# Performance work log

Measured on AMD Instinct MI355X. Metric: run time of the kernel, lower is better.

The kernel has to match this reference:

```python
import jax, jax.numpy as jnp
import numpy as np

N_HEAD = 8
N_INPUTS = 2
N_EMBD = 256
B, T1, T2 = 4, 8192, 8192


def setup_inputs() -> dict:
    key = jax.random.key(0)
    ks = jax.random.split(key, 8)
    s = 1.0 / np.sqrt(N_EMBD)
    return {
        "x": jax.random.normal(ks[0], (B, T1, N_EMBD), dtype=jnp.float32),
        "y": jax.random.normal(ks[1], (N_INPUTS, B, T2, N_EMBD), dtype=jnp.float32),
        "Wq": jax.random.normal(ks[2], (N_EMBD, N_EMBD), dtype=jnp.float32) * s,
        "bq": jnp.zeros((N_EMBD,), dtype=jnp.float32),
        "Wk": jax.random.normal(ks[3], (N_INPUTS, N_EMBD, N_EMBD), dtype=jnp.float32) * s,
        "bk": jnp.zeros((N_INPUTS, N_EMBD), dtype=jnp.float32),
        "Wv": jax.random.normal(ks[4], (N_INPUTS, N_EMBD, N_EMBD), dtype=jnp.float32) * s,
        "bv": jnp.zeros((N_INPUTS, N_EMBD), dtype=jnp.float32),
        "Wp": jax.random.normal(ks[5], (N_EMBD, N_EMBD), dtype=jnp.float32) * s,
        "bp": jnp.zeros((N_EMBD,), dtype=jnp.float32),
    }


def _split_heads(t):
    # [B, T, C] -> [B, H, T, d]
    Bt, Tt, C = t.shape
    return t.reshape(Bt, Tt, N_HEAD, C // N_HEAD).transpose(0, 2, 1, 3)


def reference(x, y, Wq, bq, Wk, bk, Wv, bv, Wp, bp):
    Bx, T, C = x.shape
    q = jax.nn.softmax(_split_heads(x @ Wq + bq), axis=-1)  # [B,H,T1,d]
    out = q  # faithful to original: out initialized to q
    for i in range(N_INPUTS):
        k = jax.nn.softmax(_split_heads(y[i] @ Wk[i] + bk[i]), axis=-1)  # [B,H,T2,d]
        v = _split_heads(y[i] @ Wv[i] + bv[i])                            # [B,H,T2,d]
        k_cumsum = k.sum(axis=-2, keepdims=True)                          # [B,H,1,d]
        D_inv = 1.0 / (q * k_cumsum).sum(axis=-1, keepdims=True)          # [B,H,T1,1]
        kv = jnp.einsum('bhtd,bhte->bhde', k, v)                          # [B,H,d,d]
        out = out + jnp.einsum('bhnd,bhde->bhne', q, kv) * D_inv
    # b h n d -> b n (h d)
    out = out.transpose(0, 2, 1, 3).reshape(Bx, T, C)
    return out @ Wp + bp
```

## Files before the change

### kernel.cpp

```cpp
#include <hip/hip_runtime.h>
#include <math.h>

#define NHEAD 8
#define CEMB  256
#define NIN   2
#define BB    4
#define TT    8192

typedef __attribute__((ext_vector_type(8))) short short8;
typedef __attribute__((ext_vector_type(4))) float f32x4;
typedef __attribute__((ext_vector_type(16))) float f32x16;

__device__ __forceinline__ unsigned short f2bf(float f) {
    union { float f; unsigned u; } v; v.f = f;
    unsigned u = v.u;
    return (unsigned short)((u + 0x7fffu + ((u >> 16) & 1u)) >> 16);
}
__device__ __forceinline__ float bf2f(unsigned short s) {
    union { unsigned u; float f; } v; v.u = ((unsigned)s) << 16;
    return v.f;
}

__global__ __launch_bounds__(256) void prep_w(const float* __restrict__ Wq,
    const float* __restrict__ Wk, const float* __restrict__ Wv,
    const float* __restrict__ Wp, unsigned short* __restrict__ wsb)
{
    int gid = blockIdx.x * 256 + threadIdx.x;
    int m = gid >> 16;
    int idx = gid & 65535;
    int n = idx >> 8, k = idx & 255;
    const float* src; unsigned short* dst;
    switch (m) {
        case 0: src = Wq;          dst = wsb;          break;
        case 1: src = Wk;          dst = wsb + 65536;  break;
        case 2: src = Wk + 65536;  dst = wsb + 131072; break;
        case 3: src = Wv;          dst = wsb + 196608; break;
        case 4: src = Wv + 65536;  dst = wsb + 262144; break;
        default: src = Wp;         dst = wsb + 327680; break;
    }
    dst[n * 256 + k] = f2bf(src[k * 256 + n]);
}

__global__ __launch_bounds__(512, 4) void passA(const float* __restrict__ y,
    const float* __restrict__ bk, const float* __restrict__ bv,
    const unsigned short* __restrict__ Wkt, const unsigned short* __restrict__ Wvt,
    float* __restrict__ part)
{
    __shared__ unsigned short ytile[64][256];
    __shared__ unsigned short tr[8][32][64];

    const int i = blockIdx.z, b = blockIdx.y, x0 = blockIdx.x;
    const int tid = threadIdx.x;
    const int wid = tid >> 6, lane = tid & 63;
    const int lg = lane >> 4, li = lane & 15;
    const int l31 = lane & 31, hk = lane >> 5;
    const int h = wid, lm = li & 7;

    const float bk0 = bk[i * CEMB + h * 32 + li];
    const float bk1 = bk[i * CEMB + h * 32 + 16 + li];
    const float bv0 = bv[i * CEMB + h * 32 + li];
    const float bv1 = bv[i * CEMB + h * 32 + 16 + li];

    f32x16 kvacc = {};
    float ksa0 = 0.f, ksa1 = 0.f;

    for (int iter = 0; iter < 2; ++iter) {
        __syncthreads();
        const int row0 = x0 * 128 + iter * 64;
        const float* yb = y + ((size_t)(i * BB + b) * TT + row0) * CEMB;
        #pragma unroll
        for (int j = 0; j < 8; ++j) {
            int idx = tid + j * 512;
            int r = idx >> 6, c4 = (idx & 63) << 2;
            int sw = ((((c4 >> 3) ^ (r & 7)) << 3) | (c4 & 7));
            float4 v4 = *(const float4*)&yb[(size_t)r * CEMB + c4];
            ushort4 p; p.x = f2bf(v4.x); p.y = f2bf(v4.y); p.z = f2bf(v4.z); p.w = f2bf(v4.w);
            *(ushort4*)&ytile[r][sw] = p;
        }
        __syncthreads();

        f32x4 acc[4][2];
        #pragma unroll
        for (int rt = 0; rt < 4; ++rt) { acc[rt][0] = (f32x4){}; acc[rt][1] = (f32x4){}; }
        {
            const unsigned short* wk0 = Wkt + ((size_t)(i * 256 + h * 32 + li)) * 256 + lg * 8;
            const unsigned short* wk1 = wk0 + 16 * 256;
            #pragma unroll 2
            for (int ks = 0; ks < 8; ++ks) {
                const int sw8 = (((4 * ks + lg) ^ lm) << 3);
                short8 a0 = *(const short8*)&ytile[li][sw8];
                short8 a1 = *(const short8*)&ytile[16 + li][sw8];
                short8 a2 = *(const short8*)&ytile[32 + li][sw8];
                short8 a3 = *(const short8*)&ytile[48 + li][sw8];
                short8 f0 = *(const short8*)(wk0 + ks * 32);
                short8 f1 = *(const short8*)(wk1 + ks * 32);
                acc[0][0] = __builtin_amdgcn_mfma_f32_16x16x32_bf16(a0, f0, acc[0][0], 0, 0, 0);
                acc[0][1] = __builtin_amdgcn_mfma_f32_16x16x32_bf16(a0, f1, acc[0][1], 0, 0, 0);
                acc[1][0] = __builtin_amdgcn_mfma_f32_16x16x32_bf16(a1, f0, acc[1][0], 0, 0, 0);
                acc[1][1] = __builtin_amdgcn_mfma_f32_16x16x32_bf16(a1, f1, acc[1][1], 0, 0, 0);
                acc[2][0] = __builtin_amdgcn_mfma_f32_16x16x32_bf16(a2, f0, acc[2][0], 0, 0, 0);
                acc[2][1] = __builtin_amdgcn_mfma_f32_16x16x32_bf16(a2, f1, acc[2][1], 0, 0, 0);
                acc[3][0] = __builtin_amdgcn_mfma_f32_16x16x32_bf16(a3, f0, acc[3][0], 0, 0, 0);
                acc[3][1] = __builtin_amdgcn_mfma_f32_16x16x32_bf16(a3, f1, acc[3][1], 0, 0, 0);
            }
        }
        #pragma unroll
        for (int rt = 0; rt < 4; ++rt) {
            float kq0[4], kq1[4];
            #pragma unroll
            for (int reg = 0; reg < 4; ++reg) {
                float l0 = acc[rt][0][reg] + bk0;
                float l1 = acc[rt][1][reg] + bk1;
                float m = fmaxf(l0, l1);
                m = fmaxf(m, __shfl_xor(m, 1, 16));
                m = fmaxf(m, __shfl_xor(m, 2, 16));
                m = fmaxf(m, __shfl_xor(m, 4, 16));
                m = fmaxf(m, __shfl_xor(m, 8, 16));
                float e0 = __expf(l0 - m), e1 = __expf(l1 - m);
                float s = e0 + e1;
                s += __shfl_xor(s, 1, 16);
                s += __shfl_xor(s, 2, 16);
                s += __shfl_xor(s, 4, 16);
                s += __shfl_xor(s, 8, 16);
                float isv = 1.f / s;
                kq0[reg] = e0 * isv; kq1[reg] = e1 * isv;
                ksa0 += kq0[reg]; ksa1 += kq1[reg];
            }
            const int wof = ((((2 * rt + (lg >> 1)) ^ lm) << 3) | ((lg & 1) << 2));
            ushort4 p;
            p.x = f2bf(kq0[0]); p.y = f2bf(kq0[1]); p.z = f2bf(kq0[2]); p.w = f2bf(kq0[3]);
            *(ushort4*)&tr[wid][li][wof] = p;
            p.x = f2bf(kq1[0]); p.y = f2bf(kq1[1]); p.z = f2bf(kq1[2]); p.w = f2bf(kq1[3]);
            *(ushort4*)&tr[wid][16 + li][wof] = p;
        }
        #pragma unroll
        for (int rt = 0; rt < 4; ++rt) { acc[rt][0] = (f32x4){}; acc[rt][1] = (f32x4){}; }
        {
            const unsigned short* wv0 = Wvt + ((size_t)(i * 256 + h * 32 + li)) * 256 + lg * 8;
            const unsigned short* wv1 = wv0 + 16 * 256;
            #pragma unroll 2
            for (int ks = 0; ks < 8; ++ks) {
                const int sw8 = (((4 * ks + lg) ^ lm) << 3);
                short8 a0 = *(const short8*)&ytile[li][sw8];
                short8 a1 = *(const short8*)&ytile[16 + li][sw8];
                short8 a2 = *(const short8*)&ytile[32 + li][sw8];
                short8 a3 = *(const short8*)&ytile[48 + li][sw8];
                short8 f0 = *(const short8*)(wv0 + ks * 32);
                short8 f1 = *(const short8*)(wv1 + ks * 32);
                acc[0][0] = __builtin_amdgcn_mfma_f32_16x16x32_bf16(a0, f0, acc[0][0], 0, 0, 0);
                acc[0][1] = __builtin_amdgcn_mfma_f32_16x16x32_bf16(a0, f1, acc[0][1], 0, 0, 0);
                acc[1][0] = __builtin_amdgcn_mfma_f32_16x16x32_bf16(a1, f0, acc[1][0], 0, 0, 0);
                acc[1][1] = __builtin_amdgcn_mfma_f32_16x16x32_bf16(a1, f1, acc[1][1], 0, 0, 0);
                acc[2][0] = __builtin_amdgcn_mfma_f32_16x16x32_bf16(a2, f0, acc[2][0], 0, 0, 0);
                acc[2][1] = __builtin_amdgcn_mfma_f32_16x16x32_bf16(a2, f1, acc[2][1], 0, 0, 0);
                acc[3][0] = __builtin_amdgcn_mfma_f32_16x16x32_bf16(a3, f0, acc[3][0], 0, 0, 0);
                acc[3][1] = __builtin_amdgcn_mfma_f32_16x16x32_bf16(a3, f1, acc[3][1], 0, 0, 0);
            }
        }
        asm volatile("s_waitcnt lgkmcnt(0)" ::: "memory");
        short8 ka[4];
        #pragma unroll
        for (int ts = 0; ts < 4; ++ts) {
            const int tof = (((2 * ts + hk) ^ (l31 & 7)) << 3);
            ka[ts] = *(const short8*)&tr[wid][l31][tof];
        }
        asm volatile("s_waitcnt lgkmcnt(0)" ::: "memory");
        #pragma unroll
        for (int rt = 0; rt < 4; ++rt) {
            const int wof = ((((2 * rt + (lg >> 1)) ^ lm) << 3) | ((lg & 1) << 2));
            ushort4 p;
            p.x = f2bf(acc[rt][0][0] + bv0); p.y = f2bf(acc[rt][0][1] + bv0);
            p.z = f2bf(acc[rt][0][2] + bv0); p.w = f2bf(acc[rt][0][3] + bv0);
            *(ushort4*)&tr[wid][li][wof] = p;
            p.x = f2bf(acc[rt][1][0] + bv1); p.y = f2bf(acc[rt][1][1] + bv1);
            p.z = f2bf(acc[rt][1][2] + bv1); p.w = f2bf(acc[rt][1][3] + bv1);
            *(ushort4*)&tr[wid][16 + li][wof] = p;
        }
        asm volatile("s_waitcnt lgkmcnt(0)" ::: "memory");
        #pragma unroll
        for (int ts = 0; ts < 4; ++ts) {
            const int tof = (((2 * ts + hk) ^ (l31 & 7)) << 3);
            short8 vb = *(const short8*)&tr[wid][l31][tof];
            kvacc = __builtin_amdgcn_mfma_f32_32x32x16_bf16(ka[ts], vb, kvacc, 0, 0, 0);
        }
    }

    const size_t slot = (size_t)(i * BB + b) * 64 + x0;
    float* pb = part + slot * (NHEAD * 1056) + (size_t)h * 1056;
    #pragma unroll
    for (int reg = 0; reg < 16; ++reg) {
        int d = (reg & 3) + 8 * (reg >> 2) + 4 * hk;
        pb[d * 32 + l31] = kvacc[reg];
    }
    float s0 = ksa0, s1 = ksa1;
    s0 += __shfl_xor(s0, 16, 64); s0 += __shfl_xor(s0, 32, 64);
    s1 += __shfl_xor(s1, 16, 64); s1 += __shfl_xor(s1, 32, 64);
    if (lg == 0) { pb[1024 + li] = s0; pb[1024 + 16 + li] = s1; }
}

__global__ __launch_bounds__(256) void reduceKV(const float* __restrict__ part,
    unsigned short* __restrict__ kvt, float* __restrict__ ksum)
{
    const int g = blockIdx.y, ech = blockIdx.x;
    const int ib = g >> 3, h = g & 7;
    const int tid = threadIdx.x;
    const int e0 = ech * 264;
    const int e1 = (e0 + 264 < 1056) ? e0 + 264 : 1056;
    for (int e = e0 + tid; e < e1; e += 256) {
        float s = 0.f;
        const float* p = part + ((size_t)ib * 64 * NHEAD + h) * 1056 + e;
        #pragma unroll 4
        for (int xx = 0; xx < 64; ++xx) s += p[(size_t)xx * NHEAD * 1056];
        if (e < 1024) kvt[(size_t)g * 1024 + (e & 31) * 32 + (e >> 5)] = f2bf(s);
        else          ksum[(size_t)g * 32 + (e - 1024)] = s;
    }
}

__global__ __launch_bounds__(512, 4) void passB(const float* __restrict__ x,
    const float* __restrict__ bq, const float* __restrict__ bp,
    const unsigned short* __restrict__ Wqt, const unsigned short* __restrict__ Wpt,
    const unsigned short* __restrict__ kvt, const float* __restrict__ ksum,
    float* __restrict__ out)
{
    __shared__ unsigned short xa[64][256];
    __shared__ unsigned short ql[64][256];
    __shared__ float dl[2][64][8];

    const int b = blockIdx.y, x0 = blockIdx.x;
    const int row0 = x0 * 64;
    const int tid = threadIdx.x;
    const int wid = tid >> 6, lane = tid & 63, lg = lane >> 4, li = lane & 15;
    const int h = wid, lm = li & 7;

    const float* xb = x + ((size_t)b * TT + row0) * CEMB;
    #pragma unroll
    for (int j = 0; j < 8; ++j) {
        int idx = tid + j * 512;
        int r = idx >> 6, c4 = (idx & 63) << 2;
        int sw = ((((c4 >> 3) ^ (r & 7)) << 3) | (c4 & 7));
        float4 v4 = *(const float4*)&xb[(size_t)r * CEMB + c4];
        ushort4 p; p.x = f2bf(v4.x); p.y = f2bf(v4.y); p.z = f2bf(v4.z); p.w = f2bf(v4.w);
        *(ushort4*)&xa[r][sw] = p;
    }
    __syncthreads();

    {
        f32x4 qa[4][2];
        #pragma unroll
        for (int rt = 0; rt < 4; ++rt) { qa[rt][0] = (f32x4){}; qa[rt][1] = (f32x4){}; }

        const unsigned short* wq0 = Wqt + ((size_t)(h * 32 + li)) * 256 + lg * 8;
        const unsigned short* wq1 = wq0 + 16 * 256;
        #pragma unroll 2
        for (int ks = 0; ks < 8; ++ks) {
            const int sw8 = (((4 * ks + lg) ^ lm) << 3);
            short8 a0 = *(const short8*)&xa[li][sw8];
            short8 a1 = *(const short8*)&xa[16 + li][sw8];
            short8 a2 = *(const short8*)&xa[32 + li][sw8];
            short8 a3 = *(const short8*)&xa[48 + li][sw8];
            short8 f0 = *(const short8*)(wq0 + ks * 32);
            short8 f1 = *(const short8*)(wq1 + ks * 32);
            qa[0][0] = __builtin_amdgcn_mfma_f32_16x16x32_bf16(a0, f0, qa[0][0], 0, 0, 0);
            qa[0][1] = __builtin_amdgcn_mfma_f32_16x16x32_bf16(a0, f1, qa[0][1], 0, 0, 0);
            qa[1][0] = __builtin_amdgcn_mfma_f32_16x16x32_bf16(a1, f0, qa[1][0], 0, 0, 0);
            qa[1][1] = __builtin_amdgcn_mfma_f32_16x16x32_bf16(a1, f1, qa[1][1], 0, 0, 0);
            qa[2][0] = __builtin_amdgcn_mfma_f32_16x16x32_bf16(a2, f0, qa[2][0], 0, 0, 0);
            qa[2][1] = __builtin_amdgcn_mfma_f32_16x16x32_bf16(a2, f1, qa[2][1], 0, 0, 0);
            qa[3][0] = __builtin_amdgcn_mfma_f32_16x16x32_bf16(a3, f0, qa[3][0], 0, 0, 0);
            qa[3][1] = __builtin_amdgcn_mfma_f32_16x16x32_bf16(a3, f1, qa[3][1], 0, 0, 0);
        }
        const float bq0 = bq[h * 32 + li];
        const float bq1 = bq[h * 32 + 16 + li];
        #pragma unroll
        for (int rt = 0; rt < 4; ++rt) {
            #pragma unroll
            for (int reg = 0; reg < 4; ++reg) {
                float l0 = qa[rt][0][reg] + bq0;
                float l1 = qa[rt][1][reg] + bq1;
                float m = fmaxf(l0, l1);
                m = fmaxf(m, __shfl_xor(m, 1, 16));
                m = fmaxf(m, __shfl_xor(m, 2, 16));
                m = fmaxf(m, __shfl_xor(m, 4, 16));
                m = fmaxf(m, __shfl_xor(m, 8, 16));
                float e0 = __expf(l0 - m), e1 = __expf(l1 - m);
                float s = e0 + e1;
                s += __shfl_xor(s, 1, 16);
                s += __shfl_xor(s, 2, 16);
                s += __shfl_xor(s, 4, 16);
                s += __shfl_xor(s, 8, 16);
                float isv = 1.f / s;
                int r = 16 * rt + 4 * lg + reg;
                int r7 = r & 7;
                int sw0 = (((4 * h + (li >> 3)) ^ r7) << 3) | lm;
                int sw1 = (((4 * h + 2 + (li >> 3)) ^ r7) << 3) | lm;
                ql[r][sw0] = f2bf(e0 * isv);
                ql[r][sw1] = f2bf(e1 * isv);
            }
        }
    }
    __syncthreads();

    {
        int r = tid >> 3, hh = tid & 7;
        const float* ks0 = ksum + ((size_t)(0 * BB + b) * 8 + hh) * 32;
        const float* ks1 = ksum + ((size_t)(1 * BB + b) * 8 + hh) * 32;
        float s0 = 0.f, s1 = 0.f;
        #pragma unroll
        for (int d8 = 0; d8 < 4; ++d8) {
            int cu = (((4 * hh + d8) ^ (r & 7)) << 3);
            #pragma unroll
            for (int dd = 0; dd < 8; ++dd) {
                float qv = bf2f(ql[r][cu + dd]);
                s0 += qv * ks0[d8 * 8 + dd];
                s1 += qv * ks1[d8 * 8 + dd];
            }
        }
        dl[0][r][hh] = 1.f / s0;
        dl[1][r][hh] = 1.f / s1;
    }
    __syncthreads();

    #pragma unroll
    for (int rt = 0; rt < 4; ++rt) {
        float of0[4], of1[4];
        #pragma unroll
        for (int reg = 0; reg < 4; ++reg) {
            int rk = (4 * lg + reg) & 7;
            int r = 16 * rt + 4 * lg + reg;
            int col0 = (((4 * h + (li >> 3)) ^ rk) << 3) | lm;
            int col1 = (((4 * h + 2 + (li >> 3)) ^ rk) << 3) | lm;
            of0[reg] = bf2f(ql[r][col0]);
            of1[reg] = bf2f(ql[r][col1]);
        }
        short8 af = *(const short8*)&ql[16 * rt + li][(((4 * h + lg) ^ lm) << 3)];
        #pragma unroll
        for (int ii = 0; ii < NIN; ++ii) {
            const unsigned short* kvb = kvt + ((size_t)((ii * BB + b) * 8 + h)) * 1024;
            short8 b0 = *(const short8*)(kvb + (size_t)li * 32 + lg * 8);
            short8 b1 = *(const short8*)(kvb + (size_t)(16 + li) * 32 + lg * 8);
            f32x4 z = {};
            f32x4 t0 = __builtin_amdgcn_mfma_f32_16x16x32_bf16(af, b0, z, 0, 0, 0);
            f32x4 t1 = __builtin_amdgcn_mfma_f32_16x16x32_bf16(af, b1, z, 0, 0, 0);
            #pragma unroll
            for (int reg = 0; reg < 4; ++reg) {
                float dv = dl[ii][16 * rt + 4 * lg + reg][h];
                of0[reg] += t0[reg] * dv;
                of1[reg] += t1[reg] * dv;
            }
        }
        #pragma unroll
        for (int reg = 0; reg < 4; ++reg) {
            int rk = (4 * lg + reg) & 7;
            int r = 16 * rt + 4 * lg + reg;
            int col0 = (((4 * h + (li >> 3)) ^ rk) << 3) | lm;
            int col1 = (((4 * h + 2 + (li >> 3)) ^ rk) << 3) | lm;
            xa[r][col0] = f2bf(of0[reg]);
            xa[r][col1] = f2bf(of1[reg]);
        }
    }
    __syncthreads();

    {
        f32x4 of[4][2];
        #pragma unroll
        for (int rt = 0; rt < 4; ++rt) { of[rt][0] = (f32x4){}; of[rt][1] = (f32x4){}; }
        const unsigned short* wp0 = Wpt + ((size_t)(h * 32 + li)) * 256 + lg * 8;
        const unsigned short* wp1 = wp0 + 16 * 256;
        #pragma unroll 2
        for (int ks = 0; ks < 8; ++ks) {
            const int sw8 = (((4 * ks + lg) ^ lm) << 3);
            short8 a0 = *(const short8*)&xa[li][sw8];
            short8 a1 = *(const short8*)&xa[16 + li][sw8];
            short8 a2 = *(const short8*)&xa[32 + li][sw8];
            short8 a3 = *(const short8*)&xa[48 + li][sw8];
            short8 f0 = *(const short8*)(wp0 + ks * 32);
            short8 f1 = *(const short8*)(wp1 + ks * 32);
            of[0][0] = __builtin_amdgcn_mfma_f32_16x16x32_bf16(a0, f0, of[0][0], 0, 0, 0);
            of[0][1] = __builtin_amdgcn_mfma_f32_16x16x32_bf16(a0, f1, of[0][1], 0, 0, 0);
            of[1][0] = __builtin_amdgcn_mfma_f32_16x16x32_bf16(a1, f0, of[1][0], 0, 0, 0);
            of[1][1] = __builtin_amdgcn_mfma_f32_16x16x32_bf16(a1, f1, of[1][1], 0, 0, 0);
            of[2][0] = __builtin_amdgcn_mfma_f32_16x16x32_bf16(a2, f0, of[2][0], 0, 0, 0);
            of[2][1] = __builtin_amdgcn_mfma_f32_16x16x32_bf16(a2, f1, of[2][1], 0, 0, 0);
            of[3][0] = __builtin_amdgcn_mfma_f32_16x16x32_bf16(a3, f0, of[3][0], 0, 0, 0);
            of[3][1] = __builtin_amdgcn_mfma_f32_16x16x32_bf16(a3, f1, of[3][1], 0, 0, 0);
        }
        const float bp0 = bp[h * 32 + li];
        const float bp1 = bp[h * 32 + 16 + li];
        #pragma unroll
        for (int rt = 0; rt < 4; ++rt) {
            #pragma unroll
            for (int reg = 0; reg < 4; ++reg) {
                int r = 16 * rt + 4 * lg + reg;
                float* ob = out + ((size_t)b * TT + row0 + r) * CEMB + h * 32;
                ob[li]      = of[rt][0][reg] + bp0;
                ob[16 + li] = of[rt][1][reg] + bp1;
            }
        }
    }
}

extern "C" void kernel_launch(void* const* d_in, const int* in_sizes, int n_in,
                              void* d_out, int out_size, void* d_ws, size_t ws_size,
                              hipStream_t stream)
{
    const float* x  = (const float*)d_in[0];
    const float* y  = (const float*)d_in[1];
    const float* Wq = (const float*)d_in[2];
    const float* bq = (const float*)d_in[3];
    const float* Wk = (const float*)d_in[4];
    const float* bk = (const float*)d_in[5];
    const float* Wv = (const float*)d_in[6];
    const float* bv = (const float*)d_in[7];
    const float* Wp = (const float*)d_in[8];
    const float* bp = (const float*)d_in[9];
    float* out = (float*)d_out;

    unsigned short* wsb = (unsigned short*)d_ws;
    float* part = (float*)((char*)d_ws + 786432);
    unsigned short* kvt = (unsigned short*)((char*)d_ws + 18087936);
    float* ksum = (float*)((char*)d_ws + 18219008);

    hipLaunchKernelGGL(prep_w, dim3(1536), dim3(256), 0, stream, Wq, Wk, Wv, Wp, wsb);
    hipLaunchKernelGGL(passA, dim3(64, BB, NIN), dim3(512), 0, stream,
                       y, bk, bv, wsb + 65536, wsb + 196608, part);
    hipLaunchKernelGGL(reduceKV, dim3(4, 64), dim3(256), 0, stream, part, kvt, ksum);
    hipLaunchKernelGGL(passB, dim3(128, BB), dim3(512), 0, stream,
                       x, bq, bp, wsb + 0, wsb + 327680, kvt, ksum, out);
}
```

Before: 126.4 us.

## Split passA row tile into 32-row halves to cut registers and transpose LDS

Each 64-row y tile in passA is now processed in two 32-row halves, so a wave holds four 16x16 accumulators per projection instead of eight, and the transpose buffer shrinks from 64 to 36 columns per row (padded, no XOR swizzle). The goal is lower register pressure and LDS footprint, which may allow more resident waves, and the weight pointers are hoisted out of the loop. The cost is more LDS round trips and waitcnt/sched_barrier points per tile. The padded layout may also change bank-conflict behaviour compared with the swizzled one.

```diff
diff --git a/kernel.cpp b/kernel.cpp
--- a/kernel.cpp
+++ b/kernel.cpp
@@ -47,7 +47,7 @@
     float* __restrict__ part)
 {
     __shared__ unsigned short ytile[64][256];
-    __shared__ unsigned short tr[8][32][64];
+    __shared__ unsigned short tr[8][32][36];
 
     const int i = blockIdx.z, b = blockIdx.y, x0 = blockIdx.x;
     const int tid = threadIdx.x;
@@ -60,6 +60,11 @@
     const float bk1 = bk[i * CEMB + h * 32 + 16 + li];
     const float bv0 = bv[i * CEMB + h * 32 + li];
     const float bv1 = bv[i * CEMB + h * 32 + 16 + li];
+
+    const unsigned short* wk0 = Wkt + ((size_t)(i * 256 + h * 32 + li)) * 256 + lg * 8;
+    const unsigned short* wk1 = wk0 + 16 * 256;
+    const unsigned short* wv0 = Wvt + ((size_t)(i * 256 + h * 32 + li)) * 256 + lg * 8;
+    const unsigned short* wv1 = wv0 + 16 * 256;
 
     f32x16 kvacc = {};
     float ksa0 = 0.f, ksa1 = 0.f;
@@ -79,109 +84,93 @@
         }
         __syncthreads();
 
-        f32x4 acc[4][2];
-        #pragma unroll
-        for (int rt = 0; rt < 4; ++rt) { acc[rt][0] = (f32x4){}; acc[rt][1] = (f32x4){}; }
-        {
-            const unsigned short* wk0 = Wkt + ((size_t)(i * 256 + h * 32 + li)) * 256 + lg * 8;
-            const unsigned short* wk1 = wk0 + 16 * 256;
-            #pragma unroll 2
+        #pragma unroll
+        for (int rh = 0; rh < 2; ++rh) {
+            const int R0 = rh * 32;
+            f32x4 acc00 = {}, acc01 = {}, acc10 = {}, acc11 = {};
+            #pragma unroll
             for (int ks = 0; ks < 8; ++ks) {
                 const int sw8 = (((4 * ks + lg) ^ lm) << 3);
-                short8 a0 = *(const short8*)&ytile[li][sw8];
-                short8 a1 = *(const short8*)&ytile[16 + li][sw8];
-                short8 a2 = *(const short8*)&ytile[32 + li][sw8];
-                short8 a3 = *(const short8*)&ytile[48 + li][sw8];
+                short8 a0 = *(const short8*)&ytile[R0 + li][sw8];
+                short8 a1 = *(const short8*)&ytile[R0 + 16 + li][sw8];
                 short8 f0 = *(const short8*)(wk0 + ks * 32);
                 short8 f1 = *(const short8*)(wk1 + ks * 32);
-                acc[0][0] = __builtin_amdgcn_mfma_f32_16x16x32_bf16(a0, f0, acc[0][0], 0, 0, 0);
-                acc[0][1] = __builtin_amdgcn_mfma_f32_16x16x32_bf16(a0, f1, acc[0][1], 0, 0, 0);
-                acc[1][0] = __builtin_amdgcn_mfma_f32_16x16x32_bf16(a1, f0, acc[1][0], 0, 0, 0);
-                acc[1][1] = __builtin_amdgcn_mfma_f32_16x16x32_bf16(a1, f1, acc[1][1], 0, 0, 0);
-                acc[2][0] = __builtin_amdgcn_mfma_f32_16x16x32_bf16(a2, f0, acc[2][0], 0, 0, 0);
-                acc[2][1] = __builtin_amdgcn_mfma_f32_16x16x32_bf16(a2, f1, acc[2][1], 0, 0, 0);
-                acc[3][0] = __builtin_amdgcn_mfma_f32_16x16x32_bf16(a3, f0, acc[3][0], 0, 0, 0);
-                acc[3][1] = __builtin_amdgcn_mfma_f32_16x16x32_bf16(a3, f1, acc[3][1], 0, 0, 0);
-            }
-        }
-        #pragma unroll
-        for (int rt = 0; rt < 4; ++rt) {
-            float kq0[4], kq1[4];
-            #pragma unroll
-            for (int reg = 0; reg < 4; ++reg) {
-                float l0 = acc[rt][0][reg] + bk0;
-                float l1 = acc[rt][1][reg] + bk1;
-                float m = fmaxf(l0, l1);
-                m = fmaxf(m, __shfl_xor(m, 1, 16));
-                m = fmaxf(m, __shfl_xor(m, 2, 16));
-                m = fmaxf(m, __shfl_xor(m, 4, 16));
-                m = fmaxf(m, __shfl_xor(m, 8, 16));
-                float e0 = __expf(l0 - m), e1 = __expf(l1 - m);
-                float s = e0 + e1;
-                s += __shfl_xor(s, 1, 16);
-                s += __shfl_xor(s, 2, 16);
-                s += __shfl_xor(s, 4, 16);
-                s += __shfl_xor(s, 8, 16);
-                float isv = 1.f / s;
-                kq0[reg] = e0 * isv; kq1[reg] = e1 * isv;
-                ksa0 += kq0[reg]; ksa1 += kq1[reg];
-            }
-            const int wof = ((((2 * rt + (lg >> 1)) ^ lm) << 3) | ((lg & 1) << 2));
-            ushort4 p;
-            p.x = f2bf(kq0[0]); p.y = f2bf(kq0[1]); p.z = f2bf(kq0[2]); p.w = f2bf(kq0[3]);
-            *(ushort4*)&tr[wid][li][wof] = p;
-            p.x = f2bf(kq1[0]); p.y = f2bf(kq1[1]); p.z = f2bf(kq1[2]); p.w = f2bf(kq1[3]);
-            *(ushort4*)&tr[wid][16 + li][wof] = p;
-        }
-        #pragma unroll
-        for (int rt = 0; rt < 4; ++rt) { acc[rt][0] = (f32x4){}; acc[rt][1] = (f32x4){}; }
-        {
-            const unsigned short* wv0 = Wvt + ((size_t)(i * 256 + h * 32 + li)) * 256 + lg * 8;
-            const unsigned short* wv1 = wv0 + 16 * 256;
-            #pragma unroll 2
+                acc00 = __builtin_amdgcn_mfma_f32_16x16x32_bf16(a0, f0, acc00, 0, 0, 0);
+                acc01 = __builtin_amdgcn_mfma_f32_16x16x32_bf16(a0, f1, acc01, 0, 0, 0);
+                acc10 = __builtin_amdgcn_mfma_f32_16x16x32_bf16(a1, f0, acc10, 0, 0, 0);
+                acc11 = __builtin_amdgcn_mfma_f32_16x16x32_bf16(a1, f1, acc11, 0, 0, 0);
+            }
+            #pragma unroll
+            for (int rt = 0; rt < 2; ++rt) {
+                f32x4 A0 = rt ? acc10 : acc00;
+                f32x4 A1 = rt ? acc11 : acc01;
+                float kq0[4], kq1[4];
+                #pragma unroll
+                for (int reg = 0; reg < 4; ++reg) {
+                    float l0 = A0[reg] + bk0;
+                    float l1 = A1[reg] + bk1;
+                    float m = fmaxf(l0, l1);
+                    m = fmaxf(m, __shfl_xor(m, 1, 16));
+                    m = fmaxf(m, __shfl_xor(m, 2, 16));
+                    m = fmaxf(m, __shfl_xor(m, 4, 16));
+                    m = fmaxf(m, __shfl_xor(m, 8, 16));
+                    float e0 = __expf(l0 - m), e1 = __expf(l1 - m);
+                    float s = e0 + e1;
+                    s += __shfl_xor(s, 1, 16);
+                    s += __shfl_xor(s, 2, 16);
+                    s += __shfl_xor(s, 4, 16);
+                    s += __shfl_xor(s, 8, 16);
+                    float isv = 1.f / s;
+                    kq0[reg] = e0 * isv; kq1[reg] = e1 * isv;
+                    ksa0 += kq0[reg]; ksa1 += kq1[reg];
+                }
+                ushort4 p;
+                p.x = f2bf(kq0[0]); p.y = f2bf(kq0[1]); p.z = f2bf(kq0[2]); p.w = f2bf(kq0[3]);
+                *(ushort4*)&tr[wid][li][16 * rt + 4 * lg] = p;
+                p.x = f2bf(kq1[0]); p.y = f2bf(kq1[1]); p.z = f2bf(kq1[2]); p.w = f2bf(kq1[3]);
+                *(ushort4*)&tr[wid][16 + li][16 * rt + 4 * lg] = p;
+            }
+            acc00 = (f32x4){}; acc01 = (f32x4){}; acc10 = (f32x4){}; acc11 = (f32x4){};
+            #pragma unroll
             for (int ks = 0; ks < 8; ++ks) {
                 const int sw8 = (((4 * ks + lg) ^ lm) << 3);
-                short8 a0 = *(const short8*)&ytile[li][sw8];
-                short8 a1 = *(const short8*)&ytile[16 + li][sw8];
-                short8 a2 = *(const short8*)&ytile[32 + li][sw8];
-                short8 a3 = *(const short8*)&ytile[48 + li][sw8];
+                short8 a0 = *(const short8*)&ytile[R0 + li][sw8];
+                short8 a1 = *(const short8*)&ytile[R0 + 16 + li][sw8];
                 short8 f0 = *(const short8*)(wv0 + ks * 32);
                 short8 f1 = *(const short8*)(wv1 + ks * 32);
-                acc[0][0] = __builtin_amdgcn_mfma_f32_16x16x32_bf16(a0, f0, acc[0][0], 0, 0, 0);
-                acc[0][1] = __builtin_amdgcn_mfma_f32_16x16x32_bf16(a0, f1, acc[0][1], 0, 0, 0);
-                acc[1][0] = __builtin_amdgcn_mfma_f32_16x16x32_bf16(a1, f0, acc[1][0], 0, 0, 0);
-                acc[1][1] = __builtin_amdgcn_mfma_f32_16x16x32_bf16(a1, f1, acc[1][1], 0, 0, 0);
-                acc[2][0] = __builtin_amdgcn_mfma_f32_16x16x32_bf16(a2, f0, acc[2][0], 0, 0, 0);
-                acc[2][1] = __builtin_amdgcn_mfma_f32_16x16x32_bf16(a2, f1, acc[2][1], 0, 0, 0);
-                acc[3][0] = __builtin_amdgcn_mfma_f32_16x16x32_bf16(a3, f0, acc[3][0], 0, 0, 0);
-                acc[3][1] = __builtin_amdgcn_mfma_f32_16x16x32_bf16(a3, f1, acc[3][1], 0, 0, 0);
-            }
-        }
-        asm volatile("s_waitcnt lgkmcnt(0)" ::: "memory");
-        short8 ka[4];
-        #pragma unroll
-        for (int ts = 0; ts < 4; ++ts) {
-            const int tof = (((2 * ts + hk) ^ (l31 & 7)) << 3);
-            ka[ts] = *(const short8*)&tr[wid][l31][tof];
-        }
-        asm volatile("s_waitcnt lgkmcnt(0)" ::: "memory");
-        #pragma unroll
-        for (int rt = 0; rt < 4; ++rt) {
-            const int wof = ((((2 * rt + (lg >> 1)) ^ lm) << 3) | ((lg & 1) << 2));
-            ushort4 p;
-            p.x = f2bf(acc[rt][0][0] + bv0); p.y = f2bf(acc[rt][0][1] + bv0);
-            p.z = f2bf(acc[rt][0][2] + bv0); p.w = f2bf(acc[rt][0][3] + bv0);
-            *(ushort4*)&tr[wid][li][wof] = p;
-            p.x = f2bf(acc[rt][1][0] + bv1); p.y = f2bf(acc[rt][1][1] + bv1);
-            p.z = f2bf(acc[rt][1][2] + bv1); p.w = f2bf(acc[rt][1][3] + bv1);
-            *(ushort4*)&tr[wid][16 + li][wof] = p;
-        }
-        asm volatile("s_waitcnt lgkmcnt(0)" ::: "memory");
-        #pragma unroll
-        for (int ts = 0; ts < 4; ++ts) {
-            const int tof = (((2 * ts + hk) ^ (l31 & 7)) << 3);
-            short8 vb = *(const short8*)&tr[wid][l31][tof];
-            kvacc = __builtin_amdgcn_mfma_f32_32x32x16_bf16(ka[ts], vb, kvacc, 0, 0, 0);
+                acc00 = __builtin_amdgcn_mfma_f32_16x16x32_bf16(a0, f0, acc00, 0, 0, 0);
+                acc01 = __builtin_amdgcn_mfma_f32_16x16x32_bf16(a0, f1, acc01, 0, 0, 0);
+                acc10 = __builtin_amdgcn_mfma_f32_16x16x32_bf16(a1, f0, acc10, 0, 0, 0);
+                acc11 = __builtin_amdgcn_mfma_f32_16x16x32_bf16(a1, f1, acc11, 0, 0, 0);
+            }
+            asm volatile("s_waitcnt lgkmcnt(0)" ::: "memory");
+            __builtin_amdgcn_sched_barrier(0);
+            short8 ka0 = *(const short8*)&tr[wid][l31][hk * 8];
+            short8 ka1 = *(const short8*)&tr[wid][l31][16 + hk * 8];
+            asm volatile("s_waitcnt lgkmcnt(0)" ::: "memory");
+            __builtin_amdgcn_sched_barrier(0);
+            #pragma unroll
+            for (int rt = 0; rt < 2; ++rt) {
+                f32x4 A0 = rt ? acc10 : acc00;
+                f32x4 A1 = rt ? acc11 : acc01;
+                ushort4 p;
+                p.x = f2bf(A0[0] + bv0); p.y = f2bf(A0[1] + bv0);
+                p.z = f2bf(A0[2] + bv0); p.w = f2bf(A0[3] + bv0);
+                *(ushort4*)&tr[wid][li][16 * rt + 4 * lg] = p;
+                p.x = f2bf(A1[0] + bv1); p.y = f2bf(A1[1] + bv1);
+                p.z = f2bf(A1[2] + bv1); p.w = f2bf(A1[3] + bv1);
+                *(ushort4*)&tr[wid][16 + li][16 * rt + 4 * lg] = p;
+            }
+            asm volatile("s_waitcnt lgkmcnt(0)" ::: "memory");
+            __builtin_amdgcn_sched_barrier(0);
+            {
+                short8 vb0 = *(const short8*)&tr[wid][l31][hk * 8];
+                short8 vb1 = *(const short8*)&tr[wid][l31][16 + hk * 8];
+                kvacc = __builtin_amdgcn_mfma_f32_32x32x16_bf16(ka0, vb0, kvacc, 0, 0, 0);
+                kvacc = __builtin_amdgcn_mfma_f32_32x32x16_bf16(ka1, vb1, kvacc, 0, 0, 0);
+            }
+            asm volatile("s_waitcnt lgkmcnt(0)" ::: "memory");
+            __builtin_amdgcn_sched_barrier(0);
         }
     }
 
```

New measurement: 194.1 us. 1.54x slower.
